# Kernel tuning notes

Hardware: AMD Instinct MI355X
Metric: run time of the kernel (lower is better)

Reference implementation:

```python
import jax, jax.numpy as jnp
import numpy as np

BATCH, T, N = 64, 512, 1024

def setup_inputs() -> dict:
    key = jax.random.key(0)
    k1, k2, k3 = jax.random.split(key, 3)
    input_sequence = jax.random.normal(k1, (BATCH, T, N), dtype=jnp.float32)
    W_self_lower = jax.random.normal(k2, (N, N), dtype=jnp.float32) * 0.1
    W_input = jax.random.normal(k3, (N, N), dtype=jnp.float32) * 0.1
    return {"input_sequence": input_sequence, "W_self_lower": W_self_lower, "W_input": W_input}

def reference(input_sequence, W_self_lower, W_input):
    # W_self symmetric: (W + W.T)/2; note W_self.T == W_self
    W_self = (W_self_lower + W_self_lower.T) * 0.5
    batch = input_sequence.shape[0]
    n = W_self.shape[0]
    # Precompute input projection for all timesteps: (B, T, N) @ (N, N)^T
    x_proj = jnp.einsum('btn,mn->btm', input_sequence, W_input)
    h0 = jnp.zeros((batch, n), dtype=input_sequence.dtype)

    def step(h, xp_t):
        h_new = jnp.tanh(h @ W_self.T + xp_t)
        return h_new, h_new

    # scan over time axis: move T to leading axis
    _, states = jax.lax.scan(step, h0, jnp.swapaxes(x_proj, 0, 1))
    return jnp.swapaxes(states, 0, 1)  # (B, T, N)
```

## Files before the change

### kernel.cpp

```cpp
#include <hip/hip_runtime.h>
#include <cstdint>
#include <cmath>

constexpr int BATCH = 64;
constexpr int T     = 512;
constexpr int N     = 1024;
constexpr int NWG   = 256;
constexpr int NG    = 16;
constexpr int GM    = 32;

typedef float f4 __attribute__((ext_vector_type(4)));
typedef float f2 __attribute__((ext_vector_type(2)));

struct alignas(128) PadInt { int v; int pad[31]; };
__device__ PadInt g_cnt[NG];
__device__ PadInt g_flag[NG];

__device__ __forceinline__ f4 ld_sys_x4(const float* p) {
  f4 v;
  asm volatile("global_load_dwordx4 %0, %1, off sc0 sc1" : "=v"(v) : "v"(p));
  return v;
}
__device__ __forceinline__ int ld_sys_i32(const int* p) {
  int v;
  asm volatile("global_load_dword %0, %1, off sc0 sc1\n\ts_waitcnt vmcnt(0)"
               : "=v"(v) : "v"(p) : "memory");
  return v;
}
__device__ __forceinline__ void st_sys_x2(float* p, f2 v) {
  asm volatile("global_store_dwordx2 %0, %1, off sc0 sc1 nt" ::"v"(p), "v"(v)
               : "memory");
}
__device__ __forceinline__ void wait_vm0(void) {
  asm volatile("s_waitcnt vmcnt(0)" ::: "memory");
  __builtin_amdgcn_sched_barrier(0);
}

__device__ __forceinline__ void arrive_cnt(int bg, int t) {
  int old = __hip_atomic_fetch_add(&g_cnt[bg].v, 1, __ATOMIC_RELAXED,
                                   __HIP_MEMORY_SCOPE_AGENT);
  if (old == t * GM + (GM - 1))
    __hip_atomic_store(&g_flag[bg].v, t + 1, __ATOMIC_RELAXED,
                       __HIP_MEMORY_SCOPE_AGENT);
}
__device__ __forceinline__ void pollf(int bg, int e) {
  while (ld_sys_i32(&g_flag[bg].v) < e) __builtin_amdgcn_s_sleep(1);
}

__global__ __launch_bounds__(256) void symm_k(const float* __restrict__ W,
                                              float* __restrict__ Ws) {
  if (blockIdx.x == 0 && blockIdx.y == 0 && threadIdx.x < NG) {
    __hip_atomic_store(&g_cnt[threadIdx.x].v, 0, __ATOMIC_RELAXED,
                       __HIP_MEMORY_SCOPE_AGENT);
    __hip_atomic_store(&g_flag[threadIdx.x].v, 0, __ATOMIC_RELAXED,
                       __HIP_MEMORY_SCOPE_AGENT);
  }
  int j = blockIdx.x * 16 + (threadIdx.x & 15);
  int i = blockIdx.y * 16 + (threadIdx.x >> 4);
  Ws[(size_t)i * N + j] = 0.5f * (W[(size_t)i * N + j] + W[(size_t)j * N + i]);
}

__global__ __launch_bounds__(256) void xproj_gemm(const float* __restrict__ A,
                                                  const float* __restrict__ B,
                                                  float* __restrict__ C,
                                                  int M) {
  constexpr int BM = 128, BN = 128, BK = 16;
  __shared__ float As[BK][BM + 4];
  __shared__ float Bs[BK][BN + 4];

  const int tid = threadIdx.x;
  const int lin = blockIdx.x + gridDim.x * blockIdx.y;
  const int sw  = ((lin & 7) << 8) + (lin >> 3);
  const int bm  = sw >> 3;
  const int bn  = sw & 7;
  const int tx = tid & 15, ty = tid >> 4;
  const int K = N;

  float acc[8][8];
#pragma unroll
  for (int i = 0; i < 8; ++i)
#pragma unroll
    for (int j = 0; j < 8; ++j) acc[i][j] = 0.f;

  for (int kt = 0; kt < K; kt += BK) {
#pragma unroll
    for (int s = 0; s < 2; ++s) {
      int f = tid + s * 256;
      int row = f >> 2, kq = f & 3;
      float4 a = *reinterpret_cast<const float4*>(
          &A[(size_t)(bm * BM + row) * K + kt + kq * 4]);
      As[kq * 4 + 0][row] = a.x;
      As[kq * 4 + 1][row] = a.y;
      As[kq * 4 + 2][row] = a.z;
      As[kq * 4 + 3][row] = a.w;
      float4 b = *reinterpret_cast<const float4*>(
          &B[(size_t)(bn * BN + row) * K + kt + kq * 4]);
      Bs[kq * 4 + 0][row] = b.x;
      Bs[kq * 4 + 1][row] = b.y;
      Bs[kq * 4 + 2][row] = b.z;
      Bs[kq * 4 + 3][row] = b.w;
    }
    __syncthreads();

#pragma unroll
    for (int k = 0; k < BK; ++k) {
      float a[8], b[8];
      *reinterpret_cast<float4*>(&a[0]) =
          *reinterpret_cast<const float4*>(&As[k][ty * 8]);
      *reinterpret_cast<float4*>(&a[4]) =
          *reinterpret_cast<const float4*>(&As[k][ty * 8 + 4]);
      *reinterpret_cast<float4*>(&b[0]) =
          *reinterpret_cast<const float4*>(&Bs[k][tx * 8]);
      *reinterpret_cast<float4*>(&b[4]) =
          *reinterpret_cast<const float4*>(&Bs[k][tx * 8 + 4]);
#pragma unroll
      for (int i = 0; i < 8; ++i)
#pragma unroll
        for (int j = 0; j < 8; ++j) acc[i][j] = fmaf(a[i], b[j], acc[i][j]);
    }
    __syncthreads();
  }

#pragma unroll
  for (int i = 0; i < 8; ++i) {
    size_t row = (size_t)bm * BM + ty * 8 + i;
#pragma unroll
    for (int j = 0; j < 8; j += 4) {
      *reinterpret_cast<float4*>(&C[row * N + bn * BN + tx * 8 + j]) =
          *reinterpret_cast<const float4*>(&acc[i][j]);
    }
  }
}

__global__ __launch_bounds__(384, 1) void rnn_persist(
    float* __restrict__ out, const float* __restrict__ Ws) {
  const int tid = threadIdx.x;
  const int wg  = blockIdx.x;
  const int p   = wg & 7;
  const int cg  = wg >> 3;
  const int m0  = cg * 32;
  const int gA  = 2 * p, gB = 2 * p + 1;
  const int b0A = gA * 4, b0B = gB * 4;
  const size_t TN = (size_t)T * N;

  __shared__ __align__(16) char lds_raw[84992];
  __shared__ int lflags[64];
  float (*hA)[1028] = reinterpret_cast<float(*)[1028]>(lds_raw);
  float (*hB)[1028] = reinterpret_cast<float(*)[1028]>(lds_raw + 16448);
  float* xplA = reinterpret_cast<float*>(lds_raw + 32896);
  float* xplB = reinterpret_cast<float*>(lds_raw + 33408);
  float (*Wq)[1028] = reinterpret_cast<float(*)[1028]>(lds_raw);

  if (tid == 0) {
    lflags[0] = -1; lflags[16] = -1; lflags[32] = 0; lflags[48] = 0;
  }
  __syncthreads();

  const int l  = tid & 63;
  const int v  = tid >> 6;
  const int c2 = l & 3;
  const int kp = l >> 2;
  const int clocal = v * 8 + c2 * 2;

  f4 wreg[2][16];
  for (int quarter = 0; quarter < 4; ++quarter) {
    if (tid < 256) {
#pragma unroll
      for (int q = 0; q < 8; ++q)
        *reinterpret_cast<float4*>(&Wq[q][tid * 4]) =
            *reinterpret_cast<const float4*>(
                &Ws[(size_t)(m0 + quarter * 8 + q) * N + tid * 4]);
    }
    __syncthreads();
    if (v == quarter) {
#pragma unroll
      for (int ci = 0; ci < 2; ++ci)
#pragma unroll
        for (int j = 0; j < 16; ++j)
          wreg[ci][j] =
              *reinterpret_cast<const f4*>(&Wq[c2 * 2 + ci][kp * 4 + 64 * j]);
    }
    __syncthreads();
  }

  if (tid < 256) {
    float* obA[4];
    float* obB[4];
#pragma unroll
    for (int bi = 0; bi < 4; ++bi) {
      obA[bi] = out + (size_t)(b0A + bi) * TN + m0 + clocal;
      obB[bi] = out + (size_t)(b0B + bi) * TN + m0 + clocal;
    }

    auto do_chain = [&](float (*hX)[1028], float* xplX, int rdy_idx,
                        int cnt_idx, float* const* obX, int t) {
      while (*(volatile int*)&lflags[rdy_idx] < t) __builtin_amdgcn_s_sleep(1);
      __builtin_amdgcn_fence(__ATOMIC_ACQUIRE, "workgroup");
      float acc[8];
#pragma unroll
      for (int i = 0; i < 8; ++i) acc[i] = 0.f;
      if (t > 0) {
#pragma unroll
        for (int j = 0; j < 16; ++j) {
          const int kb = kp * 4 + 64 * j;
          f4 hv[4];
#pragma unroll
          for (int bi = 0; bi < 4; ++bi)
            hv[bi] = *reinterpret_cast<const f4*>(&hX[bi][kb]);
#pragma unroll
          for (int bi = 0; bi < 4; ++bi)
#pragma unroll
            for (int ci = 0; ci < 2; ++ci) {
              float a = acc[bi * 2 + ci];
              a = fmaf(hv[bi].x, wreg[ci][j].x, a);
              a = fmaf(hv[bi].y, wreg[ci][j].y, a);
              a = fmaf(hv[bi].z, wreg[ci][j].z, a);
              a = fmaf(hv[bi].w, wreg[ci][j].w, a);
              acc[bi * 2 + ci] = a;
            }
        }
#pragma unroll
        for (int o = 4; o < 64; o <<= 1)
#pragma unroll
          for (int i = 0; i < 8; ++i) acc[i] += __shfl_xor(acc[i], o, 64);
      }
      if (kp == 0) {
#pragma unroll
        for (int bi = 0; bi < 4; ++bi) {
          float x0 = xplX[bi * 32 + clocal];
          float x1 = xplX[bi * 32 + clocal + 1];
          f2 r;
          r.x = tanhf((t > 0 ? acc[bi * 2 + 0] : 0.f) + x0);
          r.y = tanhf((t > 0 ? acc[bi * 2 + 1] : 0.f) + x1);
          st_sys_x2(obX[bi] + (size_t)t * N, r);
        }
      }
      wait_vm0();
      if (l == 0) atomicAdd(&lflags[cnt_idx], 1);
    };

    for (int t = 0; t < T; ++t) {
      do_chain(hA, xplA, 0, 32, obA, t);
      do_chain(hB, xplB, 16, 48, obB, t);
    }
  } else {
    const bool isB = (tid >= 320);
    const int lane = l;
    const int g    = isB ? gB : gA;
    const int b0   = isB ? b0B : b0A;
    float (*hb)[1028] = isB ? hB : hA;
    float* xpl = isB ? xplB : xplA;
    volatile int* ready = isB ? (volatile int*)&lflags[16]
                              : (volatile int*)&lflags[0];
    volatile int* cnt = isB ? (volatile int*)&lflags[48]
                            : (volatile int*)&lflags[32];

    const int r = lane >> 4;
    const int c = lane & 15;
    const float* hrow = out + (size_t)(b0 + r) * TN;
    const int xr = lane >> 3, xc = (lane & 7) * 4;
    const float* xsrc = out + (size_t)(b0 + xr) * TN + m0 + xc;

    {
      f4 xv;
      if (lane < 32) xv = ld_sys_x4(xsrc);
      wait_vm0();
      if (lane < 32) *reinterpret_cast<f4*>(&xpl[xr * 32 + xc]) = xv;
      __builtin_amdgcn_fence(__ATOMIC_RELEASE, "workgroup");
      if (lane == 0) *ready = 0;
    }

    for (int t = 1; t < T; ++t) {
      if (lane == 0) {
        while (*cnt < 4 * t) __builtin_amdgcn_s_sleep(1);
        arrive_cnt(g, t - 1);
        pollf(g, t);
      }
      const float* hs = hrow + (size_t)(t - 1) * N;
      f4 tmp[16];
      f4 xv;
#pragma unroll
      for (int q = 0; q < 16; ++q) tmp[q] = ld_sys_x4(hs + 4 * (c + 16 * q));
      if (lane < 32) xv = ld_sys_x4(xsrc + (size_t)t * N);
      wait_vm0();
#pragma unroll
      for (int q = 0; q < 16; ++q)
        *reinterpret_cast<f4*>(&hb[r][4 * (c + 16 * q)]) = tmp[q];
      if (lane < 32) *reinterpret_cast<f4*>(&xpl[xr * 32 + xc]) = xv;
      __builtin_amdgcn_fence(__ATOMIC_RELEASE, "workgroup");
      if (lane == 0) *ready = t;
    }
  }
}

extern "C" void kernel_launch(void* const* d_in, const int* in_sizes, int n_in,
                              void* d_out, int out_size, void* d_ws,
                              size_t ws_size, hipStream_t stream) {
  const float* in_seq  = (const float*)d_in[0];
  const float* W_lower = (const float*)d_in[1];
  const float* W_input = (const float*)d_in[2];
  float* out = (float*)d_out;
  float* Ws  = (float*)d_ws;

  symm_k<<<dim3(N / 16, N / 16), 256, 0, stream>>>(W_lower, Ws);
  xproj_gemm<<<dim3(N / 128, (BATCH * T) / 128), 256, 0, stream>>>(
      in_seq, W_input, out, BATCH * T);
  rnn_persist<<<NWG, 384, 0, stream>>>(out, Ws);
}
```

Before: 3.434 ms.

## Split batch into four 2-row chains and use per-WG flag barrier

Each workgroup now runs four independent chains of 2 batch rows instead of two chains of 4 rows, with four loader waves (512 threads) feeding them. This gives more pipelining between compute and loads. The grid-wide counter-plus-flag atomic barrier is replaced by per-workgroup flag slots: each loader writes its own step, and a whole wave polls all 32 slots of its group with one vote. This removes the serialized atomic fetch-add and the last-arriver flag hop. In exchange there is more polling traffic and smaller per-chain compute granularity.

```diff
diff --git a/kernel.cpp b/kernel.cpp
--- a/kernel.cpp
+++ b/kernel.cpp
@@ -6,15 +6,14 @@
 constexpr int T     = 512;
 constexpr int N     = 1024;
 constexpr int NWG   = 256;
-constexpr int NG    = 16;
+constexpr int NG    = 32;
 constexpr int GM    = 32;
 
 typedef float f4 __attribute__((ext_vector_type(4)));
 typedef float f2 __attribute__((ext_vector_type(2)));
 
 struct alignas(128) PadInt { int v; int pad[31]; };
-__device__ PadInt g_cnt[NG];
-__device__ PadInt g_flag[NG];
+__device__ PadInt g_wgf[NG][GM];
 
 __device__ __forceinline__ f4 ld_sys_x4(const float* p) {
   f4 v;
@@ -31,29 +30,24 @@
   asm volatile("global_store_dwordx2 %0, %1, off sc0 sc1 nt" ::"v"(p), "v"(v)
                : "memory");
 }
+__device__ __forceinline__ void st_sys_i32(int* p, int v) {
+  asm volatile("global_store_dword %0, %1, off sc0 sc1" ::"v"(p), "v"(v)
+               : "memory");
+}
 __device__ __forceinline__ void wait_vm0(void) {
   asm volatile("s_waitcnt vmcnt(0)" ::: "memory");
   __builtin_amdgcn_sched_barrier(0);
 }
 
-__device__ __forceinline__ void arrive_cnt(int bg, int t) {
-  int old = __hip_atomic_fetch_add(&g_cnt[bg].v, 1, __ATOMIC_RELAXED,
-                                   __HIP_MEMORY_SCOPE_AGENT);
-  if (old == t * GM + (GM - 1))
-    __hip_atomic_store(&g_flag[bg].v, t + 1, __ATOMIC_RELAXED,
-                       __HIP_MEMORY_SCOPE_AGENT);
-}
-__device__ __forceinline__ void pollf(int bg, int e) {
-  while (ld_sys_i32(&g_flag[bg].v) < e) __builtin_amdgcn_s_sleep(1);
-}
-
 __global__ __launch_bounds__(256) void symm_k(const float* __restrict__ W,
                                               float* __restrict__ Ws) {
-  if (blockIdx.x == 0 && blockIdx.y == 0 && threadIdx.x < NG) {
-    __hip_atomic_store(&g_cnt[threadIdx.x].v, 0, __ATOMIC_RELAXED,
-                       __HIP_MEMORY_SCOPE_AGENT);
-    __hip_atomic_store(&g_flag[threadIdx.x].v, 0, __ATOMIC_RELAXED,
-                       __HIP_MEMORY_SCOPE_AGENT);
+  if (blockIdx.x == 0 && blockIdx.y == 0) {
+#pragma unroll
+    for (int s = 0; s < 4; ++s) {
+      int idx = threadIdx.x + 256 * s;
+      __hip_atomic_store(&g_wgf[idx >> 5][idx & 31].v, -1, __ATOMIC_RELAXED,
+                         __HIP_MEMORY_SCOPE_AGENT);
+    }
   }
   int j = blockIdx.x * 16 + (threadIdx.x & 15);
   int i = blockIdx.y * 16 + (threadIdx.x >> 4);
@@ -132,34 +126,33 @@
   }
 }
 
-__global__ __launch_bounds__(384, 1) void rnn_persist(
+__global__ __launch_bounds__(512, 1) void rnn_persist(
     float* __restrict__ out, const float* __restrict__ Ws) {
   const int tid = threadIdx.x;
   const int wg  = blockIdx.x;
   const int p   = wg & 7;
   const int cg  = wg >> 3;
   const int m0  = cg * 32;
-  const int gA  = 2 * p, gB = 2 * p + 1;
-  const int b0A = gA * 4, b0B = gB * 4;
   const size_t TN = (size_t)T * N;
 
-  __shared__ __align__(16) char lds_raw[84992];
-  __shared__ int lflags[64];
-  float (*hA)[1028] = reinterpret_cast<float(*)[1028]>(lds_raw);
-  float (*hB)[1028] = reinterpret_cast<float(*)[1028]>(lds_raw + 16448);
-  float* xplA = reinterpret_cast<float*>(lds_raw + 32896);
-  float* xplB = reinterpret_cast<float*>(lds_raw + 33408);
-  float (*Wq)[1028] = reinterpret_cast<float(*)[1028]>(lds_raw);
+  __shared__ __align__(16) float hc[4][2][1028];
+  __shared__ float xpl[4][64];
+  __shared__ int lflags[128];
+  float (*Wq)[1028] = reinterpret_cast<float(*)[1028]>(&hc[0][0][0]);
 
   if (tid == 0) {
-    lflags[0] = -1; lflags[16] = -1; lflags[32] = 0; lflags[48] = 0;
+#pragma unroll
+    for (int c = 0; c < 4; ++c) {
+      lflags[c * 16] = -1;
+      lflags[64 + c * 16] = 0;
+    }
   }
   __syncthreads();
 
-  const int l  = tid & 63;
-  const int v  = tid >> 6;
+  const int l = tid & 63;
+  const int v = tid >> 6;
+  const int kp = l >> 2;
   const int c2 = l & 3;
-  const int kp = l >> 2;
   const int clocal = v * 8 + c2 * 2;
 
   f4 wreg[2][16];
@@ -183,112 +176,103 @@
     __syncthreads();
   }
 
-  if (tid < 256) {
-    float* obA[4];
-    float* obB[4];
-#pragma unroll
-    for (int bi = 0; bi < 4; ++bi) {
-      obA[bi] = out + (size_t)(b0A + bi) * TN + m0 + clocal;
-      obB[bi] = out + (size_t)(b0B + bi) * TN + m0 + clocal;
-    }
-
-    auto do_chain = [&](float (*hX)[1028], float* xplX, int rdy_idx,
-                        int cnt_idx, float* const* obX, int t) {
-      while (*(volatile int*)&lflags[rdy_idx] < t) __builtin_amdgcn_s_sleep(1);
-      __builtin_amdgcn_fence(__ATOMIC_ACQUIRE, "workgroup");
-      float acc[8];
-#pragma unroll
-      for (int i = 0; i < 8; ++i) acc[i] = 0.f;
-      if (t > 0) {
-#pragma unroll
-        for (int j = 0; j < 16; ++j) {
-          const int kb = kp * 4 + 64 * j;
-          f4 hv[4];
-#pragma unroll
-          for (int bi = 0; bi < 4; ++bi)
-            hv[bi] = *reinterpret_cast<const f4*>(&hX[bi][kb]);
-#pragma unroll
-          for (int bi = 0; bi < 4; ++bi)
+  if (v < 4) {
+    for (int t = 0; t < T; ++t) {
+#pragma unroll
+      for (int c = 0; c < 4; ++c) {
+        const int b0 = 8 * p + 2 * c;
+        while (*(volatile int*)&lflags[c * 16] < t) __builtin_amdgcn_s_sleep(1);
+        __builtin_amdgcn_fence(__ATOMIC_ACQUIRE, "workgroup");
+        float acc[4];
+#pragma unroll
+        for (int i = 0; i < 4; ++i) acc[i] = 0.f;
+        if (t > 0) {
+#pragma unroll
+          for (int j = 0; j < 16; ++j) {
+            const int kb = kp * 4 + 64 * j;
+            f4 h0 = *reinterpret_cast<const f4*>(&hc[c][0][kb]);
+            f4 h1 = *reinterpret_cast<const f4*>(&hc[c][1][kb]);
 #pragma unroll
             for (int ci = 0; ci < 2; ++ci) {
-              float a = acc[bi * 2 + ci];
-              a = fmaf(hv[bi].x, wreg[ci][j].x, a);
-              a = fmaf(hv[bi].y, wreg[ci][j].y, a);
-              a = fmaf(hv[bi].z, wreg[ci][j].z, a);
-              a = fmaf(hv[bi].w, wreg[ci][j].w, a);
-              acc[bi * 2 + ci] = a;
+              float a0 = acc[ci], a1 = acc[2 + ci];
+              a0 = fmaf(h0.x, wreg[ci][j].x, a0);
+              a0 = fmaf(h0.y, wreg[ci][j].y, a0);
+              a0 = fmaf(h0.z, wreg[ci][j].z, a0);
+              a0 = fmaf(h0.w, wreg[ci][j].w, a0);
+              a1 = fmaf(h1.x, wreg[ci][j].x, a1);
+              a1 = fmaf(h1.y, wreg[ci][j].y, a1);
+              a1 = fmaf(h1.z, wreg[ci][j].z, a1);
+              a1 = fmaf(h1.w, wreg[ci][j].w, a1);
+              acc[ci] = a0;
+              acc[2 + ci] = a1;
             }
+          }
+#pragma unroll
+          for (int o = 4; o < 64; o <<= 1)
+#pragma unroll
+            for (int i = 0; i < 4; ++i) acc[i] += __shfl_xor(acc[i], o, 64);
         }
-#pragma unroll
-        for (int o = 4; o < 64; o <<= 1)
-#pragma unroll
-          for (int i = 0; i < 8; ++i) acc[i] += __shfl_xor(acc[i], o, 64);
+        if (l < 4) {
+#pragma unroll
+          for (int bi = 0; bi < 2; ++bi) {
+            float x0 = xpl[c][bi * 32 + clocal];
+            float x1 = xpl[c][bi * 32 + clocal + 1];
+            f2 r;
+            r.x = tanhf((t > 0 ? acc[bi * 2 + 0] : 0.f) + x0);
+            r.y = tanhf((t > 0 ? acc[bi * 2 + 1] : 0.f) + x1);
+            st_sys_x2(out + (size_t)(b0 + bi) * TN + (size_t)t * N + m0 + clocal,
+                      r);
+          }
+        }
+        wait_vm0();
+        if (l == 0) atomicAdd(&lflags[64 + c * 16], 1);
       }
-      if (kp == 0) {
-#pragma unroll
-        for (int bi = 0; bi < 4; ++bi) {
-          float x0 = xplX[bi * 32 + clocal];
-          float x1 = xplX[bi * 32 + clocal + 1];
-          f2 r;
-          r.x = tanhf((t > 0 ? acc[bi * 2 + 0] : 0.f) + x0);
-          r.y = tanhf((t > 0 ? acc[bi * 2 + 1] : 0.f) + x1);
-          st_sys_x2(obX[bi] + (size_t)t * N, r);
-        }
-      }
-      wait_vm0();
-      if (l == 0) atomicAdd(&lflags[cnt_idx], 1);
-    };
-
-    for (int t = 0; t < T; ++t) {
-      do_chain(hA, xplA, 0, 32, obA, t);
-      do_chain(hB, xplB, 16, 48, obB, t);
     }
   } else {
-    const bool isB = (tid >= 320);
-    const int lane = l;
-    const int g    = isB ? gB : gA;
-    const int b0   = isB ? b0B : b0A;
-    float (*hb)[1028] = isB ? hB : hA;
-    float* xpl = isB ? xplB : xplA;
-    volatile int* ready = isB ? (volatile int*)&lflags[16]
-                              : (volatile int*)&lflags[0];
-    volatile int* cnt = isB ? (volatile int*)&lflags[48]
-                            : (volatile int*)&lflags[32];
-
-    const int r = lane >> 4;
-    const int c = lane & 15;
-    const float* hrow = out + (size_t)(b0 + r) * TN;
-    const int xr = lane >> 3, xc = (lane & 7) * 4;
+    const int c  = v - 4;
+    const int g  = 4 * p + c;
+    const int b0 = 2 * g;
+    volatile int* ready = (volatile int*)&lflags[c * 16];
+    volatile int* cnt   = (volatile int*)&lflags[64 + c * 16];
+
+    const int rr = l >> 5;
+    const int cc = l & 31;
+    const float* hrow = out + (size_t)(b0 + rr) * TN;
+    const int xr = (l >> 3) & 1, xc = (l & 7) * 4;
     const float* xsrc = out + (size_t)(b0 + xr) * TN + m0 + xc;
 
     {
       f4 xv;
-      if (lane < 32) xv = ld_sys_x4(xsrc);
+      if (l < 16) xv = ld_sys_x4(xsrc);
       wait_vm0();
-      if (lane < 32) *reinterpret_cast<f4*>(&xpl[xr * 32 + xc]) = xv;
+      if (l < 16) *reinterpret_cast<f4*>(&xpl[c][xr * 32 + xc]) = xv;
       __builtin_amdgcn_fence(__ATOMIC_RELEASE, "workgroup");
-      if (lane == 0) *ready = 0;
+      if (l == 0) *ready = 0;
     }
 
     for (int t = 1; t < T; ++t) {
-      if (lane == 0) {
+      if (l == 0) {
         while (*cnt < 4 * t) __builtin_amdgcn_s_sleep(1);
-        arrive_cnt(g, t - 1);
-        pollf(g, t);
+        st_sys_i32(&g_wgf[g][cg].v, t - 1);
+      }
+      for (;;) {
+        int fl = ld_sys_i32(&g_wgf[g][l & 31].v);
+        if (__all((l >= 32) || (fl >= t - 1))) break;
+        __builtin_amdgcn_s_sleep(1);
       }
       const float* hs = hrow + (size_t)(t - 1) * N;
-      f4 tmp[16];
+      f4 tmp[8];
       f4 xv;
 #pragma unroll
-      for (int q = 0; q < 16; ++q) tmp[q] = ld_sys_x4(hs + 4 * (c + 16 * q));
-      if (lane < 32) xv = ld_sys_x4(xsrc + (size_t)t * N);
+      for (int q = 0; q < 8; ++q) tmp[q] = ld_sys_x4(hs + 4 * (cc + 32 * q));
+      if (l < 16) xv = ld_sys_x4(xsrc + (size_t)t * N);
       wait_vm0();
 #pragma unroll
-      for (int q = 0; q < 16; ++q)
-        *reinterpret_cast<f4*>(&hb[r][4 * (c + 16 * q)]) = tmp[q];
-      if (lane < 32) *reinterpret_cast<f4*>(&xpl[xr * 32 + xc]) = xv;
+      for (int q = 0; q < 8; ++q)
+        *reinterpret_cast<f4*>(&hc[c][rr][4 * (cc + 32 * q)]) = tmp[q];
+      if (l < 16) *reinterpret_cast<f4*>(&xpl[c][xr * 32 + xc]) = xv;
       __builtin_amdgcn_fence(__ATOMIC_RELEASE, "workgroup");
-      if (lane == 0) *ready = t;
+      if (l == 0) *ready = t;
     }
   }
 }
@@ -305,5 +289,5 @@
   symm_k<<<dim3(N / 16, N / 16), 256, 0, stream>>>(W_lower, Ws);
   xproj_gemm<<<dim3(N / 128, (BATCH * T) / 128), 256, 0, stream>>>(
       in_seq, W_input, out, BATCH * T);
-  rnn_persist<<<NWG, 384, 0, stream>>>(out, Ws);
-}
+  rnn_persist<<<NWG, 512, 0, stream>>>(out, Ws);
+}
```

Result: slower. 4.089 ms (+19.1%).

## Replace two-level group barrier with blind counter arrive and overlapped chain waits

Applied to the files above, without the earlier changes.

Drops the per-group flag, so producer waves poll the global counter directly for GM*t arrivals. The last compute wave to finish a chain now performs the global arrive itself, which removes the loader wave's hop through a local counter. Compute waves also wait for chain B's readiness and the next A step after issuing their stores but before draining them, to overlap the waits with memory traffic. The risk is heavier polling traffic on the global counter from every loader lane, and subtle ordering of the fences.

```diff
diff --git a/kernel.cpp b/kernel.cpp
--- a/kernel.cpp
+++ b/kernel.cpp
@@ -14,7 +14,6 @@
 
 struct alignas(128) PadInt { int v; int pad[31]; };
 __device__ PadInt g_cnt[NG];
-__device__ PadInt g_flag[NG];
 
 __device__ __forceinline__ f4 ld_sys_x4(const float* p) {
   f4 v;
@@ -35,24 +34,15 @@
   asm volatile("s_waitcnt vmcnt(0)" ::: "memory");
   __builtin_amdgcn_sched_barrier(0);
 }
-
-__device__ __forceinline__ void arrive_cnt(int bg, int t) {
-  int old = __hip_atomic_fetch_add(&g_cnt[bg].v, 1, __ATOMIC_RELAXED,
-                                   __HIP_MEMORY_SCOPE_AGENT);
-  if (old == t * GM + (GM - 1))
-    __hip_atomic_store(&g_flag[bg].v, t + 1, __ATOMIC_RELAXED,
-                       __HIP_MEMORY_SCOPE_AGENT);
-}
-__device__ __forceinline__ void pollf(int bg, int e) {
-  while (ld_sys_i32(&g_flag[bg].v) < e) __builtin_amdgcn_s_sleep(1);
+__device__ __forceinline__ void arrive_blind(int g) {
+  __hip_atomic_fetch_add(&g_cnt[g].v, 1, __ATOMIC_RELAXED,
+                         __HIP_MEMORY_SCOPE_AGENT);
 }
 
 __global__ __launch_bounds__(256) void symm_k(const float* __restrict__ W,
                                               float* __restrict__ Ws) {
   if (blockIdx.x == 0 && blockIdx.y == 0 && threadIdx.x < NG) {
     __hip_atomic_store(&g_cnt[threadIdx.x].v, 0, __ATOMIC_RELAXED,
-                       __HIP_MEMORY_SCOPE_AGENT);
-    __hip_atomic_store(&g_flag[threadIdx.x].v, 0, __ATOMIC_RELAXED,
                        __HIP_MEMORY_SCOPE_AGENT);
   }
   int j = blockIdx.x * 16 + (threadIdx.x & 15);
@@ -183,7 +173,7 @@
     __syncthreads();
   }
 
-  if (tid < 256) {
+  if (v < 4) {
     float* obA[4];
     float* obB[4];
 #pragma unroll
@@ -192,10 +182,8 @@
       obB[bi] = out + (size_t)(b0B + bi) * TN + m0 + clocal;
     }
 
-    auto do_chain = [&](float (*hX)[1028], float* xplX, int rdy_idx,
-                        int cnt_idx, float* const* obX, int t) {
-      while (*(volatile int*)&lflags[rdy_idx] < t) __builtin_amdgcn_s_sleep(1);
-      __builtin_amdgcn_fence(__ATOMIC_ACQUIRE, "workgroup");
+    auto compute_store = [&](float (*hX)[1028], float* xplX,
+                             float* const* obX, int t) {
       float acc[8];
 #pragma unroll
       for (int i = 0; i < 8; ++i) acc[i] = 0.f;
@@ -235,13 +223,30 @@
           st_sys_x2(obX[bi] + (size_t)t * N, r);
         }
       }
+    };
+
+    while (*(volatile int*)&lflags[0] < 0) __builtin_amdgcn_s_sleep(1);
+    __builtin_amdgcn_fence(__ATOMIC_ACQUIRE, "workgroup");
+
+    for (int t = 0; t < T; ++t) {
+      compute_store(hA, xplA, obA, t);
+      while (*(volatile int*)&lflags[16] < t) __builtin_amdgcn_s_sleep(1);
+      __builtin_amdgcn_fence(__ATOMIC_ACQUIRE, "workgroup");
       wait_vm0();
-      if (l == 0) atomicAdd(&lflags[cnt_idx], 1);
-    };
-
-    for (int t = 0; t < T; ++t) {
-      do_chain(hA, xplA, 0, 32, obA, t);
-      do_chain(hB, xplB, 16, 48, obB, t);
+      if (l == 0) {
+        int old = atomicAdd(&lflags[32], 1);
+        if (old == 4 * t + 3) arrive_blind(gA);
+      }
+      compute_store(hB, xplB, obB, t);
+      if (t < T - 1) {
+        while (*(volatile int*)&lflags[0] < t + 1) __builtin_amdgcn_s_sleep(1);
+        __builtin_amdgcn_fence(__ATOMIC_ACQUIRE, "workgroup");
+      }
+      wait_vm0();
+      if (l == 0) {
+        int old = atomicAdd(&lflags[48], 1);
+        if (old == 4 * t + 3) arrive_blind(gB);
+      }
     }
   } else {
     const bool isB = (tid >= 320);
@@ -252,8 +257,6 @@
     float* xpl = isB ? xplB : xplA;
     volatile int* ready = isB ? (volatile int*)&lflags[16]
                               : (volatile int*)&lflags[0];
-    volatile int* cnt = isB ? (volatile int*)&lflags[48]
-                            : (volatile int*)&lflags[32];
 
     const int r = lane >> 4;
     const int c = lane & 15;
@@ -271,11 +274,7 @@
     }
 
     for (int t = 1; t < T; ++t) {
-      if (lane == 0) {
-        while (*cnt < 4 * t) __builtin_amdgcn_s_sleep(1);
-        arrive_cnt(g, t - 1);
-        pollf(g, t);
-      }
+      while (ld_sys_i32(&g_cnt[g].v) < GM * t) __builtin_amdgcn_s_sleep(1);
       const float* hs = hrow + (size_t)(t - 1) * N;
       f4 tmp[16];
       f4 xv;
```

Result: slower. 4.116 ms (+19.9%).
